# Kernel tuning notes

Measured on AMD Instinct MI355X. Metric: run time of the kernel, lower is better.

## Reference

```python
import jax, jax.numpy as jnp
import numpy as np
from jax import lax

# --- STE quantizers matching the torch autograd.Functions ---
@jax.custom_vjp
def binary_quantize_w(x):
    return jnp.sign(x)

def _bqw_fwd(x):
    return jnp.sign(x), None

def _bqw_bwd(_, g):
    return (g,)  # straight-through identity

binary_quantize_w.defvjp(_bqw_fwd, _bqw_bwd)

@jax.custom_vjp
def binary_quantize_a(x):
    return jnp.sign(x)

def _bqa_fwd(x):
    return jnp.sign(x), x

def _bqa_bwd(x, g):
    return (jnp.clip(2.0 - jnp.abs(2.0 * x), a_min=0.0) * g,)

binary_quantize_a.defvjp(_bqa_fwd, _bqa_bwd)

STRIDE = 1
PAD = 1

def setup_inputs() -> dict:
    key = jax.random.key(0)
    k1, k2, k3 = jax.random.split(key, 3)
    x = jax.random.normal(k1, (32, 256, 56, 56), dtype=jnp.float32)
    M = jax.random.normal(k2, (256, 256, 3, 3), dtype=jnp.float32)
    Alpha = jax.random.uniform(k3, (256, 1, 1), dtype=jnp.float32)
    return {"x": x, "M": M, "Alpha": Alpha}

def reference(x, M, Alpha):
    bw = binary_quantize_w(M)        # (O, I, kh, kw), +/-1
    ba = binary_quantize_a(x)        # (N, C, H, W), +/-1
    out = lax.conv_general_dilated(
        ba, bw,
        window_strides=(STRIDE, STRIDE),
        padding=[(PAD, PAD), (PAD, PAD)],
        dimension_numbers=("NCHW", "OIHW", "NCHW"),
    )
    # Alpha (O,1,1) broadcasts over (N, O, H, W) trailing dims -> per-channel scale
    return out * Alpha
```

## Files before the change

kernel.cpp:

```cpp
#include <hip/hip_runtime.h>
#include <stdint.h>


typedef __attribute__((ext_vector_type(16))) float floatx16;
typedef __attribute__((ext_vector_type(8)))  int   intx8;

#define N_IMG 32
#define C_IN  256
#define O_OUT 256
#define HP 58
#define WP 58
#define GPI 3136
#define APAD_POS ((size_t)N_IMG * HP * WP)
#define APAD_BYTES (APAD_POS * C_IN)
#define TPI 13
#define AL_GRAN 1072
#define WPK_STEP 49152

__device__ __forceinline__ unsigned int sgn8(float x) {
    return x > 0.f ? 0x38u : (x < 0.f ? 0xB8u : 0u);
}

__device__ __forceinline__ void glds16(const unsigned char* g, unsigned char* l) {
    __builtin_amdgcn_global_load_lds(
        (const __attribute__((address_space(1))) unsigned int*)g,
        (__attribute__((address_space(3))) unsigned int*)l, 16, 0, 0);
}

__global__ __launch_bounds__(256) void binarize_act(
    const float* __restrict__ x, unsigned char* __restrict__ apad)
{
    int bid = blockIdx.x;
    int n = bid / HP;
    int hp = bid - n * HP;
    int tid = threadIdx.x;

    unsigned char* rowp = apad + ((size_t)(n * HP + hp) * WP) * C_IN;
    uint4 z = {0u, 0u, 0u, 0u};

    if (hp == 0 || hp == HP - 1) {
#pragma unroll
        for (int j = 0; j < 4; ++j) {
            int t = tid + 256 * j;
            if (t < WP * 16) {
                int w = t >> 4, g = t & 15;
                *(uint4*)(rowp + (size_t)w * C_IN + g * 16) = z;
            }
        }
        return;
    }
    int h = hp - 1;

    __shared__ unsigned int tile[C_IN * 15];
    __shared__ unsigned int lds2[56 * 65];

    const float* xb = x + ((size_t)n * C_IN) * GPI + h * 56;
#pragma unroll
    for (int j = 0; j < 14; ++j) {
        int t = tid + 256 * j;
        int ci = t / 14;
        int w4 = t - ci * 14;
        float4 v = *(const float4*)(xb + (size_t)ci * GPI + w4 * 4);
        tile[ci * 15 + w4] = sgn8(v.x) | (sgn8(v.y) << 8) |
                             (sgn8(v.z) << 16) | (sgn8(v.w) << 24);
    }
    __syncthreads();

#pragma unroll
    for (int j = 0; j < 14; ++j) {
        int t = tid + 256 * j;
        int wlo = t & 3;
        int cq  = (t >> 2) & 63;
        int whi = t >> 8;
        int sh = wlo * 8;
        unsigned int r = 0;
#pragma unroll
        for (int i = 0; i < 4; ++i) {
            unsigned int v = tile[(cq * 4 + i) * 15 + whi];
            r |= ((v >> sh) & 0xFFu) << (8 * i);
        }
        lds2[(whi * 4 + wlo) * 65 + cq] = r;
    }
    __syncthreads();

#pragma unroll
    for (int j = 0; j < 4; ++j) {
        int t = tid + 256 * j;
        if (t < 896) {
            int w = t >> 4, g = t & 15;
            uint4 v;
            v.x = lds2[w * 65 + g * 4 + 0];
            v.y = lds2[w * 65 + g * 4 + 1];
            v.z = lds2[w * 65 + g * 4 + 2];
            v.w = lds2[w * 65 + g * 4 + 3];
            *(uint4*)(rowp + (size_t)(w + 1) * C_IN + g * 16) = v;
        }
    }
    if (tid < 32) {
        int g = tid & 15;
        int col = (tid >> 4) * (WP - 1);
        *(uint4*)(rowp + (size_t)col * C_IN + g * 16) = z;
    }
}

__global__ __launch_bounds__(64) void pack_w(
    const float* __restrict__ M, unsigned char* __restrict__ wpk)
{
    int gid = blockIdx.x * 64 + threadIdx.x;
    int o = gid >> 6;
    int c4 = (gid & 63) << 2;
    const float* mb = M + (size_t)(o * C_IN + c4) * 9;
    int oblk = o >> 5;
    int c0q = c4 >> 6;
    int dst_in = ((c4 >> 5) & 1) * 1024 + (o & 31) * 32 + (c4 & 31);
#pragma unroll
    for (int t = 0; t < 9; ++t) {
        int kh = t / 3, kw = t - 3 * (t / 3);
        unsigned int r = sgn8(mb[t]) | (sgn8(mb[9 + t]) << 8) |
                         (sgn8(mb[18 + t]) << 16) | (sgn8(mb[27 + t]) << 24);
        size_t frag = (size_t)(kh * 4 + c0q) * WPK_STEP +
                      (size_t)(kw * 8 + oblk) * 2048;
        *(unsigned int*)(wpk + frag + dst_in) = r;
    }
}

__global__ __launch_bounds__(256, 2) void bconv_gemm(
    const unsigned char* __restrict__ apad,
    const unsigned char* __restrict__ wpk,
    const float* __restrict__ alpha,
    float* __restrict__ out)
{
    __shared__ __align__(16) unsigned char Al[2][AL_GRAN * 16];

    const int tid = threadIdx.x;
    const int wv = tid >> 6, lane = tid & 63;
    const int l31 = lane & 31, hb = lane >> 5;

    const int hw = blockIdx.x;
    const int bid = (hw & 7) * 104 + (hw >> 3);

    const int img = bid / 26;
    const int rem = bid - img * 26;
    const int tl = rem >> 1, ot = rem & 1;
    const int g0 = tl << 8;
    const int h0 = g0 / 56, w0 = g0 - h0 * 56;
    const int o_base = ot << 7;
    const int Q0 = (img * HP + h0) * WP + w0;

    int al_pos[5], al_sl[5];
#pragma unroll
    for (int it = 0; it < 5; ++it) {
        int s = (it < 4) ? (tid + (it << 8)) : (tid + 816);
        int pos = s >> 2, gI = s & 3;
        al_pos[it] = pos;
        al_sl[it]  = ((gI ^ ((pos >> 1) & 3)) << 4);
    }

    const int o_half  = (wv >> 1) << 6;
    const int px_half = (wv & 1) << 7;
    const int oblk0   = (ot << 2) + ((wv >> 1) << 1);

    int pos_tab[4], pxg[4];
#pragma unroll
    for (int nt = 0; nt < 4; ++nt) {
        int px = px_half + (nt << 5) + l31;
        pxg[nt] = g0 + px;
        int pxc = (pxg[nt] < GPI) ? px : (GPI - 1 - g0);
        pos_tab[nt] = pxc + 2 * ((w0 + pxc) / 56);
    }

    floatx16 acc[2][4] = {};

    {
        const int plim = (int)APAD_POS - 1 - Q0;
        const unsigned char* asrc = apad + ((size_t)Q0 << 8);
#pragma unroll
        for (int it = 0; it < 5; ++it) {
            int p = al_pos[it] < plim ? al_pos[it] : plim;
            int dst = (it < 4) ? ((it << 8) + (wv << 6)) : (816 + (wv << 6));
            glds16(asrc + ((size_t)p << 8) + al_sl[it], &Al[0][(size_t)dst << 4]);
        }
    }
    __syncthreads();

    int cur = 0;
    for (int t = 0; t < 12; ++t) {
        union WF { uint4 q[2]; intx8 v; };
        WF wf[2][3];
        {
            const unsigned char* wb = wpk + (size_t)t * WPK_STEP + ((size_t)lane << 5);
#pragma unroll
            for (int mt = 0; mt < 2; ++mt)
#pragma unroll
                for (int kw = 0; kw < 3; ++kw) {
                    const unsigned char* p = wb + (size_t)((kw << 3) + oblk0 + mt) * 2048;
                    wf[mt][kw].q[0] = *(const uint4*)(p);
                    wf[mt][kw].q[1] = *(const uint4*)(p + 16);
                }
        }

        if (t < 11) {
            const int t1 = t + 1;
            const int kh1 = t1 >> 2, c01 = (t1 & 3) << 6;
            const int rowbase1 = Q0 + kh1 * WP;
            const int plim1 = (int)APAD_POS - 1 - rowbase1;
            const unsigned char* asrc1 = apad + (((size_t)rowbase1 << 8) + c01);
#pragma unroll
            for (int it = 0; it < 5; ++it) {
                int p = al_pos[it] < plim1 ? al_pos[it] : plim1;
                int dst = (it < 4) ? ((it << 8) + (wv << 6)) : (816 + (wv << 6));
                glds16(asrc1 + ((size_t)p << 8) + al_sl[it],
                       &Al[cur ^ 1][(size_t)dst << 4]);
            }
        }

        const unsigned char* AlC = &Al[cur][0];
#pragma unroll
        for (int kw = 0; kw < 3; ++kw) {
#pragma unroll
            for (int nt = 0; nt < 4; ++nt) {
                int pos = pos_tab[nt] + kw;
                int rb = pos << 6;
                int m3 = (pos >> 1) & 3;
                union F { uint4 q[2]; intx8 v; } bf;
                bf.q[0] = *(const uint4*)&AlC[rb + ((((hb << 1))     ^ m3) << 4)];
                bf.q[1] = *(const uint4*)&AlC[rb + ((((hb << 1) | 1) ^ m3) << 4)];
#pragma unroll
                for (int mt = 0; mt < 2; ++mt)
                    acc[mt][nt] = __builtin_amdgcn_mfma_scale_f32_32x32x64_f8f6f4(
                        wf[mt][kw].v, bf.v, acc[mt][nt],
                        0, 0,
                        0, 0x7F7F7F7F,
                        0, 0x7F7F7F7F);
            }
        }

        __syncthreads();
        cur ^= 1;
    }

#pragma unroll
    for (int mt = 0; mt < 2; ++mt) {
#pragma unroll
        for (int r = 0; r < 16; ++r) {
            int o_loc = o_half + (mt << 5) + (r & 3) + ((r >> 2) << 3) + (hb << 2);
            int o_g = o_base + o_loc;
            float a = alpha[o_g];
            float* ob = out + ((size_t)(img * O_OUT + o_g)) * GPI;
#pragma unroll
            for (int nt = 0; nt < 4; ++nt) {
                if (pxg[nt] < GPI) ob[pxg[nt]] = acc[mt][nt][r] * a;
            }
        }
    }
}

extern "C" void kernel_launch(void* const* d_in, const int* in_sizes, int n_in,
                              void* d_out, int out_size, void* d_ws, size_t ws_size,
                              hipStream_t stream) {
    const float* x     = (const float*)d_in[0];
    const float* M     = (const float*)d_in[1];
    const float* alpha = (const float*)d_in[2];
    float* out = (float*)d_out;

    unsigned char* apad = (unsigned char*)d_ws;
    unsigned char* wpk  = apad + APAD_BYTES;

    binarize_act<<<dim3(N_IMG * HP), dim3(256), 0, stream>>>(x, apad);
    pack_w<<<dim3(256), dim3(64), 0, stream>>>(M, wpk);
    bconv_gemm<<<dim3(N_IMG * TPI * 2), dim3(256), 0, stream>>>(apad, wpk, alpha, out);
}
```

Measured before the change: 284.3 us.

## Triple-buffer activation tiles with prefetch distance two and partial vmcnt waits

```diff
diff --git a/kernel.cpp b/kernel.cpp
--- a/kernel.cpp
+++ b/kernel.cpp
@@ -15,6 +15,7 @@
 #define APAD_BYTES (APAD_POS * C_IN)
 #define TPI 13
 #define AL_GRAN 1072
+#define AL_BYTES (AL_GRAN * 16)
 #define WPK_STEP 49152
 
 __device__ __forceinline__ unsigned int sgn8(float x) {
@@ -124,13 +125,29 @@
     }
 }
 
+__device__ __forceinline__ void stage_A(const unsigned char* __restrict__ apad,
+    unsigned char* lbase, int Q0, int t, const int* al_pos, const int* al_sl,
+    int wv)
+{
+    const int kh = t >> 2, c0 = (t & 3) << 6;
+    const int rowbase = Q0 + kh * WP;
+    const int plim = (int)APAD_POS - 1 - rowbase;
+    const unsigned char* asrc = apad + (((size_t)rowbase << 8) + c0);
+#pragma unroll
+    for (int it = 0; it < 5; ++it) {
+        int p = al_pos[it] < plim ? al_pos[it] : plim;
+        int dst = (it < 4) ? ((it << 8) + (wv << 6)) : (816 + (wv << 6));
+        glds16(asrc + ((size_t)p << 8) + al_sl[it], lbase + ((size_t)dst << 4));
+    }
+}
+
 __global__ __launch_bounds__(256, 2) void bconv_gemm(
     const unsigned char* __restrict__ apad,
     const unsigned char* __restrict__ wpk,
     const float* __restrict__ alpha,
     float* __restrict__ out)
 {
-    __shared__ __align__(16) unsigned char Al[2][AL_GRAN * 16];
+    __shared__ __align__(16) unsigned char Al[3][AL_BYTES];
 
     const int tid = threadIdx.x;
     const int wv = tid >> 6, lane = tid & 63;
@@ -171,19 +188,16 @@
 
     floatx16 acc[2][4] = {};
 
-    {
-        const int plim = (int)APAD_POS - 1 - Q0;
-        const unsigned char* asrc = apad + ((size_t)Q0 << 8);
-#pragma unroll
-        for (int it = 0; it < 5; ++it) {
-            int p = al_pos[it] < plim ? al_pos[it] : plim;
-            int dst = (it < 4) ? ((it << 8) + (wv << 6)) : (816 + (wv << 6));
-            glds16(asrc + ((size_t)p << 8) + al_sl[it], &Al[0][(size_t)dst << 4]);
-        }
-    }
-    __syncthreads();
-
-    int cur = 0;
+    unsigned char* Ab = &Al[0][0];
+
+    stage_A(apad, Ab,            Q0, 0, al_pos, al_sl, wv);
+    stage_A(apad, Ab + AL_BYTES, Q0, 1, al_pos, al_sl, wv);
+    asm volatile("s_waitcnt vmcnt(5)" ::: "memory");
+    __builtin_amdgcn_sched_barrier(0);
+    __builtin_amdgcn_s_barrier();
+    __builtin_amdgcn_sched_barrier(0);
+
+    int bc = 0;
     for (int t = 0; t < 12; ++t) {
         union WF { uint4 q[2]; intx8 v; };
         WF wf[2][3];
@@ -199,22 +213,13 @@
                 }
         }
 
-        if (t < 11) {
-            const int t1 = t + 1;
-            const int kh1 = t1 >> 2, c01 = (t1 & 3) << 6;
-            const int rowbase1 = Q0 + kh1 * WP;
-            const int plim1 = (int)APAD_POS - 1 - rowbase1;
-            const unsigned char* asrc1 = apad + (((size_t)rowbase1 << 8) + c01);
-#pragma unroll
-            for (int it = 0; it < 5; ++it) {
-                int p = al_pos[it] < plim1 ? al_pos[it] : plim1;
-                int dst = (it < 4) ? ((it << 8) + (wv << 6)) : (816 + (wv << 6));
-                glds16(asrc1 + ((size_t)p << 8) + al_sl[it],
-                       &Al[cur ^ 1][(size_t)dst << 4]);
-            }
-        }
-
-        const unsigned char* AlC = &Al[cur][0];
+        if (t < 10) {
+            int b2 = bc + 2; if (b2 >= 3) b2 -= 3;
+            stage_A(apad, Ab + b2 * AL_BYTES, Q0, t + 2, al_pos, al_sl, wv);
+        }
+
+        const unsigned char* AlC = Ab + bc * AL_BYTES;
+        __builtin_amdgcn_s_setprio(1);
 #pragma unroll
         for (int kw = 0; kw < 3; ++kw) {
 #pragma unroll
@@ -234,9 +239,15 @@
                         0, 0x7F7F7F7F);
             }
         }
-
-        __syncthreads();
-        cur ^= 1;
+        __builtin_amdgcn_s_setprio(0);
+
+        if (t < 11) {
+            asm volatile("s_waitcnt vmcnt(5)" ::: "memory");
+            __builtin_amdgcn_sched_barrier(0);
+            __builtin_amdgcn_s_barrier();
+            __builtin_amdgcn_sched_barrier(0);
+        }
+        bc = (bc + 1 == 3) ? 0 : bc + 1;
     }
 
 #pragma unroll
```

Result: slower. 303.9 us (+6.9%).

## Stage weights through LDS and drop activation double buffering

Applied to the files above, without the earlier changes.

```diff
diff --git a/kernel.cpp b/kernel.cpp
--- a/kernel.cpp
+++ b/kernel.cpp
@@ -15,6 +15,7 @@
 #define APAD_BYTES (APAD_POS * C_IN)
 #define TPI 13
 #define AL_GRAN 1072
+#define WL_GRAN 1536
 #define WPK_STEP 49152
 
 __device__ __forceinline__ unsigned int sgn8(float x) {
@@ -109,18 +110,16 @@
     int gid = blockIdx.x * 64 + threadIdx.x;
     int o = gid >> 6;
     int c4 = (gid & 63) << 2;
+    int c0q = c4 >> 6;
+    int c63 = c4 & 63;
     const float* mb = M + (size_t)(o * C_IN + c4) * 9;
-    int oblk = o >> 5;
-    int c0q = c4 >> 6;
-    int dst_in = ((c4 >> 5) & 1) * 1024 + (o & 31) * 32 + (c4 & 31);
 #pragma unroll
     for (int t = 0; t < 9; ++t) {
         int kh = t / 3, kw = t - 3 * (t / 3);
         unsigned int r = sgn8(mb[t]) | (sgn8(mb[9 + t]) << 8) |
                          (sgn8(mb[18 + t]) << 16) | (sgn8(mb[27 + t]) << 24);
-        size_t frag = (size_t)(kh * 4 + c0q) * WPK_STEP +
-                      (size_t)(kw * 8 + oblk) * 2048;
-        *(unsigned int*)(wpk + frag + dst_in) = r;
+        size_t dst = ((size_t)(kh * 4 + c0q) * 3 + kw) * 16384 + o * 64 + c63;
+        *(unsigned int*)(wpk + dst) = r;
     }
 }
 
@@ -130,7 +129,8 @@
     const float* __restrict__ alpha,
     float* __restrict__ out)
 {
-    __shared__ __align__(16) unsigned char Al[2][AL_GRAN * 16];
+    __shared__ __align__(16) unsigned char Al[AL_GRAN * 16];
+    __shared__ __align__(16) unsigned char Wl[WL_GRAN * 16];
 
     const int tid = threadIdx.x;
     const int wv = tid >> 6, lane = tid & 63;
@@ -155,10 +155,17 @@
         al_pos[it] = pos;
         al_sl[it]  = ((gI ^ ((pos >> 1) & 3)) << 4);
     }
+    int wl_src[6];
+#pragma unroll
+    for (int it = 0; it < 6; ++it) {
+        int s = tid + (it << 8);
+        int r = s >> 2, q = s & 3;
+        int kw = r >> 7, ol = r & 127;
+        wl_src[it] = kw * 16384 + (o_base + ol) * 64 + ((q ^ ((r >> 1) & 3)) << 4);
+    }
 
     const int o_half  = (wv >> 1) << 6;
     const int px_half = (wv & 1) << 7;
-    const int oblk0   = (ot << 2) + ((wv >> 1) << 1);
 
     int pos_tab[4], pxg[4];
 #pragma unroll
@@ -171,72 +178,53 @@
 
     floatx16 acc[2][4] = {};
 
-    {
-        const int plim = (int)APAD_POS - 1 - Q0;
-        const unsigned char* asrc = apad + ((size_t)Q0 << 8);
+    for (int t = 0; t < 12; ++t) {
+        const int kh = t >> 2, c0 = (t & 3) << 6;
+        const int rowbase = Q0 + kh * WP;
+        const int plim = (int)APAD_POS - 1 - rowbase;
+        const unsigned char* asrc = apad + (((size_t)rowbase << 8) + c0);
+        const unsigned char* wsrc = wpk + (size_t)t * WPK_STEP;
+
+        __syncthreads();
 #pragma unroll
         for (int it = 0; it < 5; ++it) {
             int p = al_pos[it] < plim ? al_pos[it] : plim;
             int dst = (it < 4) ? ((it << 8) + (wv << 6)) : (816 + (wv << 6));
-            glds16(asrc + ((size_t)p << 8) + al_sl[it], &Al[0][(size_t)dst << 4]);
-        }
-    }
-    __syncthreads();
-
-    int cur = 0;
-    for (int t = 0; t < 12; ++t) {
-        union WF { uint4 q[2]; intx8 v; };
-        WF wf[2][3];
-        {
-            const unsigned char* wb = wpk + (size_t)t * WPK_STEP + ((size_t)lane << 5);
-#pragma unroll
-            for (int mt = 0; mt < 2; ++mt)
-#pragma unroll
-                for (int kw = 0; kw < 3; ++kw) {
-                    const unsigned char* p = wb + (size_t)((kw << 3) + oblk0 + mt) * 2048;
-                    wf[mt][kw].q[0] = *(const uint4*)(p);
-                    wf[mt][kw].q[1] = *(const uint4*)(p + 16);
-                }
-        }
-
-        if (t < 11) {
-            const int t1 = t + 1;
-            const int kh1 = t1 >> 2, c01 = (t1 & 3) << 6;
-            const int rowbase1 = Q0 + kh1 * WP;
-            const int plim1 = (int)APAD_POS - 1 - rowbase1;
-            const unsigned char* asrc1 = apad + (((size_t)rowbase1 << 8) + c01);
-#pragma unroll
-            for (int it = 0; it < 5; ++it) {
-                int p = al_pos[it] < plim1 ? al_pos[it] : plim1;
-                int dst = (it < 4) ? ((it << 8) + (wv << 6)) : (816 + (wv << 6));
-                glds16(asrc1 + ((size_t)p << 8) + al_sl[it],
-                       &Al[cur ^ 1][(size_t)dst << 4]);
-            }
-        }
-
-        const unsigned char* AlC = &Al[cur][0];
+            glds16(asrc + ((size_t)p << 8) + al_sl[it], &Al[(size_t)dst << 4]);
+        }
+#pragma unroll
+        for (int it = 0; it < 6; ++it)
+            glds16(wsrc + wl_src[it], &Wl[(size_t)(tid + (it << 8)) << 4]);
+        __syncthreads();
+
 #pragma unroll
         for (int kw = 0; kw < 3; ++kw) {
+            union F { uint4 q[2]; intx8 v; };
+            F af[2];
+#pragma unroll
+            for (int mt = 0; mt < 2; ++mt) {
+                int rl = (kw << 7) + o_half + (mt << 5) + l31;
+                int m3 = (rl >> 1) & 3;
+                af[mt].q[0] = *(const uint4*)&Wl[(size_t)(rl << 6) + ((((hb << 1))     ^ m3) << 4)];
+                af[mt].q[1] = *(const uint4*)&Wl[(size_t)(rl << 6) + ((((hb << 1) | 1) ^ m3) << 4)];
+            }
 #pragma unroll
             for (int nt = 0; nt < 4; ++nt) {
                 int pos = pos_tab[nt] + kw;
                 int rb = pos << 6;
                 int m3 = (pos >> 1) & 3;
-                union F { uint4 q[2]; intx8 v; } bf;
-                bf.q[0] = *(const uint4*)&AlC[rb + ((((hb << 1))     ^ m3) << 4)];
-                bf.q[1] = *(const uint4*)&AlC[rb + ((((hb << 1) | 1) ^ m3) << 4)];
+                F bf;
+                bf.q[0] = *(const uint4*)&Al[rb + ((((hb << 1))     ^ m3) << 4)];
+                bf.q[1] = *(const uint4*)&Al[rb + ((((hb << 1) | 1) ^ m3) << 4)];
 #pragma unroll
                 for (int mt = 0; mt < 2; ++mt)
                     acc[mt][nt] = __builtin_amdgcn_mfma_scale_f32_32x32x64_f8f6f4(
-                        wf[mt][kw].v, bf.v, acc[mt][nt],
+                        af[mt].v, bf.v, acc[mt][nt],
                         0, 0,
                         0, 0x7F7F7F7F,
                         0, 0x7F7F7F7F);
             }
         }
-
-        __syncthreads();
-        cur ^= 1;
     }
 
 #pragma unroll
```

Result: faster. 263.5 us (-7.3%).
